# Performance work log

Measured on AMD Instinct MI355X. Metric: run time of the kernel, lower is better.

The kernel has to match this reference:

```python
import jax, jax.numpy as jnp
import numpy as np

B, N, C = 1, 4096, 1024
H = 16
HD = C // H  # head_dim = 64
SCALE = HD ** -0.5


def setup_inputs() -> dict:
    key = jax.random.key(0)
    k1, k2, k3, k4, k5 = jax.random.split(key, 5)
    x1 = jax.random.normal(k1, (B, N, C), dtype=jnp.float32)
    x2 = jax.random.normal(k2, (B, N, C), dtype=jnp.float32)
    # qkv: Linear(dim, 2*all_head_dim), bias=False. Stored as (in, out) for x @ W.
    W_qkv = jax.random.normal(k3, (C, 2 * H * HD), dtype=jnp.float32) * (C ** -0.5)
    # proj: Linear(all_head_dim, dim) with bias
    W_proj = jax.random.normal(k4, (H * HD, C), dtype=jnp.float32) * ((H * HD) ** -0.5)
    b_proj = jax.random.normal(k5, (C,), dtype=jnp.float32) * 0.01
    return {"x1": x1, "x2": x2, "W_qkv": W_qkv, "W_proj": W_proj, "b_proj": b_proj}


def reference(x1, x2, W_qkv, W_proj, b_proj):
    b, n, c = x1.shape
    # qk projection: (B,N,2*H*HD) -> (2,B,H,N,HD)
    qkv = (x1 @ W_qkv).reshape(b, n, 2, H, HD).transpose(2, 0, 3, 1, 4)
    q, k = qkv[0], qkv[1]  # (B,H,N,HD)
    # V2: reshape (N,1,H,HD) then permute -> (1,H,N,HD); valid since B==1
    v = x2.reshape(n, 1, H, HD).transpose(1, 2, 0, 3)
    attn = jax.nn.softmax(jnp.einsum('bhnd,bhmd->bhnm', q * SCALE, k), axis=-1)
    out = jnp.einsum('bhnm,bhmd->bhnd', attn, v)  # broadcasts v over batch
    out = out.transpose(0, 2, 1, 3).reshape(b, n, H * HD)
    return out @ W_proj + b_proj
```

## Files before the change

### kernel.cpp

```cpp
#include <hip/hip_runtime.h>

typedef unsigned short u16;
typedef unsigned int u32;

#define HNUM 16
#define NSEQ 4096
#define CDIM 1024
#define SCALE 0.125f
#define LOG2E 1.4426950408889634f

using bf16x8 = __attribute__((ext_vector_type(8))) __bf16;
using f32x4  = __attribute__((ext_vector_type(4))) float;
using u32x4  = __attribute__((ext_vector_type(4))) u32;

__device__ __forceinline__ u16 f2bf(float f) {
  union { float f; u32 u; } v; v.f = f;
  u32 u = v.u;
  return (u16)((u + 0x7fffu + ((u >> 16) & 1u)) >> 16);
}
__device__ __forceinline__ float fexp2(float x) { return __builtin_amdgcn_exp2f(x); }

__device__ __forceinline__ f32x4 mfma16(bf16x8 a, bf16x8 b, f32x4 c) {
  return __builtin_amdgcn_mfma_f32_16x16x32_bf16(a, b, c, 0, 0, 0);
}

__device__ __forceinline__ u32 pack2(float a, float b) {
  union { float f; u32 u; } A, B;
  A.f = a; B.f = b;
  return __builtin_amdgcn_perm(B.u + 0x8000u, A.u + 0x8000u, 0x07060302u);
}

__device__ __forceinline__ void g2l16(const void* g, void* l) {
  __builtin_amdgcn_global_load_lds(
      (const __attribute__((address_space(1))) unsigned int*)(unsigned long long)g,
      (__attribute__((address_space(3))) unsigned int*)(unsigned int)(unsigned long long)l,
      16, 0, 0);
}

__device__ __forceinline__ void cvtT_body(const float* __restrict__ in,
                                          u16* __restrict__ out, int R, int C,
                                          int bx, int by, float scale, int tid) {
  __shared__ u16 t[64][65];
  const int r0 = by * 64, c0 = bx * 64;
  const int tr = tid >> 2, tc = (tid & 3) * 16;
  const float* src = in + (r0 + tr) * C + c0 + tc;
#pragma unroll
  for (int i = 0; i < 16; ++i) t[tr][tc + i] = f2bf(src[i] * scale);
  __syncthreads();
  u16* dst = out + (c0 + tr) * R + r0 + tc;
#pragma unroll
  for (int i = 0; i < 16; ++i) dst[i] = t[tc + i][tr];
}

__global__ __launch_bounds__(256) void prep_k(const float* __restrict__ x1,
                                              u16* __restrict__ x1b,
                                              const float* __restrict__ Wqkv,
                                              u16* __restrict__ WqT,
                                              const float* __restrict__ Wproj,
                                              u16* __restrict__ WpT,
                                              const float* __restrict__ x2,
                                              u16* __restrict__ Vt,
                                              float cfac) {
  const int b = blockIdx.x, tid = threadIdx.x;
  if (b < 2048) {
    const int i = (b * 256 + tid) * 8;
    const float4 f0 = *(const float4*)(x1 + i);
    const float4 f1 = *(const float4*)(x1 + i + 4);
    u32 d[4] = {pack2(f0.x, f0.y), pack2(f0.z, f0.w),
                pack2(f1.x, f1.y), pack2(f1.z, f1.w)};
    *(bf16x8*)(x1b + i) = *(bf16x8*)d;
  } else if (b < 2560) {
    const int rel = b - 2048;
    const int bx = rel & 31, by = rel >> 5;
    cvtT_body(Wqkv, WqT, 1024, 2048, bx, by, bx < 16 ? cfac : 1.0f, tid);
  } else if (b < 2816) {
    const int rel = b - 2560;
    const int bx = rel & 15, by = rel >> 4;
    cvtT_body(Wproj, WpT, 1024, 1024, bx, by, 1.0f, tid);
  } else {
    const int rel = b - 2816;
    const int bx = rel & 15, by = rel >> 4;
    cvtT_body(x2, Vt, 4096, 1024, bx, by, 1.0f, tid);
  }
}

__global__ __launch_bounds__(256) void gemm1_k(const u16* __restrict__ A,
                                               const u16* __restrict__ Bt,
                                               u16* __restrict__ C,
                                               int M, int N, int K) {
  __shared__ __align__(16) u16 As[2][128 * 64];
  __shared__ __align__(16) u16 Bs[2][128 * 64];
  const int tid = threadIdx.x;
  const int wave = tid >> 6, lane = tid & 63;
  const int quad = lane >> 4, l16 = lane & 15;
  const int m0 = blockIdx.y * 128, n0 = blockIdx.x * 128;
  const int wm = wave * 32;
  const int lrow = lane >> 3, lc8 = (lane & 7) * 8;

  f32x4 acc[2][8] = {};
#pragma unroll
  for (int c = 0; c < 4; ++c) {
    const int cw = wave * 4 + c;
    g2l16(A + (m0 + cw * 8 + lrow) * K + lc8, (char*)As[0] + cw * 1024);
    g2l16(Bt + (n0 + cw * 8 + lrow) * K + lc8, (char*)Bs[0] + cw * 1024);
  }
  const int NIT = K / 64;
  for (int it = 0; it < NIT; ++it) {
    const int cur = it & 1;
    __syncthreads();
    if (it + 1 < NIT) {
      const int k0 = (it + 1) * 64;
#pragma unroll
      for (int c = 0; c < 4; ++c) {
        const int cw = wave * 4 + c;
        g2l16(A + (m0 + cw * 8 + lrow) * K + k0 + lc8, (char*)As[1 - cur] + cw * 1024);
        g2l16(Bt + (n0 + cw * 8 + lrow) * K + k0 + lc8, (char*)Bs[1 - cur] + cw * 1024);
      }
    }
#pragma unroll
    for (int ks = 0; ks < 2; ++ks) {
      bf16x8 a[2], b[8];
#pragma unroll
      for (int mt = 0; mt < 2; ++mt)
        a[mt] = *(const bf16x8*)(As[cur] + (wm + mt * 16 + l16) * 64 + ks * 32 + quad * 8);
#pragma unroll
      for (int nt = 0; nt < 8; ++nt)
        b[nt] = *(const bf16x8*)(Bs[cur] + (nt * 16 + l16) * 64 + ks * 32 + quad * 8);
#pragma unroll
      for (int mt = 0; mt < 2; ++mt)
#pragma unroll
        for (int nt = 0; nt < 8; ++nt)
          acc[mt][nt] = mfma16(a[mt], b[nt], acc[mt][nt]);
    }
  }
#pragma unroll
  for (int mt = 0; mt < 2; ++mt)
#pragma unroll
    for (int nt = 0; nt < 8; ++nt)
#pragma unroll
      for (int r = 0; r < 4; ++r)
        C[(m0 + wm + mt * 16 + quad * 4 + r) * N + n0 + nt * 16 + l16] =
            f2bf(acc[mt][nt][r]);
}

__global__ __launch_bounds__(256) void gemm2_k(const u16* __restrict__ A,
                                               const u16* __restrict__ Bt,
                                               float* __restrict__ C,
                                               const float* __restrict__ bias,
                                               int M, int N, int K) {
  __shared__ __align__(16) u16 As[2][128 * 64];
  __shared__ __align__(16) u16 Bs[2][64 * 64];
  const int tid = threadIdx.x;
  const int wave = tid >> 6, lane = tid & 63;
  const int quad = lane >> 4, l16 = lane & 15;
  const int m0 = blockIdx.y * 128, n0 = blockIdx.x * 64;
  const int wm = wave * 32;
  const int lrow = lane >> 3, lc8 = (lane & 7) * 8;

  f32x4 acc[2][4] = {};
#pragma unroll
  for (int c = 0; c < 4; ++c) {
    const int cw = wave * 4 + c;
    g2l16(A + (m0 + cw * 8 + lrow) * K + lc8, (char*)As[0] + cw * 1024);
  }
#pragma unroll
  for (int c = 0; c < 2; ++c) {
    const int cw = wave * 2 + c;
    g2l16(Bt + (n0 + cw * 8 + lrow) * K + lc8, (char*)Bs[0] + cw * 1024);
  }
  const int NIT = K / 64;
  for (int it = 0; it < NIT; ++it) {
    const int cur = it & 1;
    __syncthreads();
    if (it + 1 < NIT) {
      const int k0 = (it + 1) * 64;
#pragma unroll
      for (int c = 0; c < 4; ++c) {
        const int cw = wave * 4 + c;
        g2l16(A + (m0 + cw * 8 + lrow) * K + k0 + lc8, (char*)As[1 - cur] + cw * 1024);
      }
#pragma unroll
      for (int c = 0; c < 2; ++c) {
        const int cw = wave * 2 + c;
        g2l16(Bt + (n0 + cw * 8 + lrow) * K + k0 + lc8, (char*)Bs[1 - cur] + cw * 1024);
      }
    }
#pragma unroll
    for (int ks = 0; ks < 2; ++ks) {
      bf16x8 a[2], b[4];
#pragma unroll
      for (int mt = 0; mt < 2; ++mt)
        a[mt] = *(const bf16x8*)(As[cur] + (wm + mt * 16 + l16) * 64 + ks * 32 + quad * 8);
#pragma unroll
      for (int nt = 0; nt < 4; ++nt)
        b[nt] = *(const bf16x8*)(Bs[cur] + (nt * 16 + l16) * 64 + ks * 32 + quad * 8);
#pragma unroll
      for (int mt = 0; mt < 2; ++mt)
#pragma unroll
        for (int nt = 0; nt < 4; ++nt)
          acc[mt][nt] = mfma16(a[mt], b[nt], acc[mt][nt]);
    }
  }
#pragma unroll
  for (int mt = 0; mt < 2; ++mt)
#pragma unroll
    for (int nt = 0; nt < 4; ++nt)
#pragma unroll
      for (int r = 0; r < 4; ++r) {
        const int col = n0 + nt * 16 + l16;
        C[(m0 + wm + mt * 16 + quad * 4 + r) * N + col] = acc[mt][nt][r] + bias[col];
      }
}

__global__ __launch_bounds__(256) void attn_k(const u16* __restrict__ QK,
                                              const u16* __restrict__ Vt,
                                              u16* __restrict__ O) {
  __shared__ __align__(16) u16 Ks[2][64 * 64];
  __shared__ __align__(16) u16 Vs[2][64 * 64];
  __shared__ __align__(16) u16 Ps[4][32 * 64];
  const int tid = threadIdx.x;
  const int wave = tid >> 6, lane = tid & 63;
  const int quad = lane >> 4, l16 = lane & 15;
  const int head = blockIdx.y;
  const int qb = blockIdx.x * 128 + wave * 32;
  const int lrow = lane >> 3;
  const int lc8 = ((lane & 7) ^ lrow) * 8;
  const int swz = (quad ^ (l16 & 7)) * 8;

  const u16* kp[2];
  const u16* vp[2];
#pragma unroll
  for (int c = 0; c < 2; ++c) {
    const int row = (wave * 2 + c) * 8 + lrow;
    kp[c] = QK + row * 2048 + CDIM + head * 64 + lc8;
    vp[c] = Vt + (head * 64 + row) * NSEQ + lc8;
  }

  bf16x8 qf[2][2];
#pragma unroll
  for (int mt = 0; mt < 2; ++mt)
#pragma unroll
    for (int ks = 0; ks < 2; ++ks)
      qf[mt][ks] = *(const bf16x8*)(QK + (qb + mt * 16 + l16) * 2048 + head * 64 +
                                    ks * 32 + quad * 8);

  union { u32x4 u; bf16x8 b; } OU;
  OU.u = (u32x4){0x3F803F80u, 0x3F803F80u, 0x3F803F80u, 0x3F803F80u};
  const bf16x8 onesf = OU.b;

  f32x4 o[2][4] = {};
  f32x4 ol[2] = {};
  u16* Pw = Ps[wave];

#pragma unroll
  for (int c = 0; c < 2; ++c) {
    const int cw = wave * 2 + c;
    g2l16(kp[c], (char*)Ks[0] + cw * 1024);
    g2l16(vp[c], (char*)Vs[0] + cw * 1024);
    kp[c] += 64 * 2048;
    vp[c] += 64;
  }

  for (int kt = 0; kt < NSEQ / 64; ++kt) {
    const int cur = kt & 1;
    __syncthreads();

    if (kt < NSEQ / 64 - 1) {
#pragma unroll
      for (int c = 0; c < 2; ++c) {
        const int cw = wave * 2 + c;
        g2l16(kp[c], (char*)Ks[1 - cur] + cw * 1024);
        g2l16(vp[c], (char*)Vs[1 - cur] + cw * 1024);
        kp[c] += 64 * 2048;
        vp[c] += 64;
      }
    }

    const u16* Kc = Ks[cur];
    const u16* Vc = Vs[cur];

    f32x4 s[2][4] = {};
#pragma unroll
    for (int ks = 0; ks < 2; ++ks)
#pragma unroll
      for (int nt = 0; nt < 4; ++nt) {
        const bf16x8 kf =
            *(const bf16x8*)(Kc + (nt * 16 + l16) * 64 + (swz ^ (ks * 32)));
#pragma unroll
        for (int mt = 0; mt < 2; ++mt)
          s[mt][nt] = mfma16(kf, qf[mt][ks], s[mt][nt]);
      }

#pragma unroll
    for (int mt = 0; mt < 2; ++mt)
#pragma unroll
      for (int nt = 0; nt < 4; ++nt) {
        const float p0 = fexp2(s[mt][nt][0]);
        const float p1 = fexp2(s[mt][nt][1]);
        const float p2 = fexp2(s[mt][nt][2]);
        const float p3 = fexp2(s[mt][nt][3]);
        u32 d01 = pack2(p0, p1), d23 = pack2(p2, p3);
        const int col8 = (nt * 2 + (quad >> 1)) ^ (l16 & 7);
        u32* dst = (u32*)(Pw + (mt * 16 + l16) * 64 + col8 * 8 + (quad & 1) * 4);
        dst[0] = d01; dst[1] = d23;
      }

#pragma unroll
    for (int ks = 0; ks < 2; ++ks) {
      bf16x8 pf[2];
#pragma unroll
      for (int mt = 0; mt < 2; ++mt)
        pf[mt] = *(const bf16x8*)(Pw + (mt * 16 + l16) * 64 + (swz ^ (ks * 32)));
#pragma unroll
      for (int dt = 0; dt < 4; ++dt) {
        const bf16x8 vf =
            *(const bf16x8*)(Vc + (dt * 16 + l16) * 64 + (swz ^ (ks * 32)));
#pragma unroll
        for (int mt = 0; mt < 2; ++mt)
          o[mt][dt] = mfma16(pf[mt], vf, o[mt][dt]);
      }
#pragma unroll
      for (int mt = 0; mt < 2; ++mt)
        ol[mt] = mfma16(pf[mt], onesf, ol[mt]);
    }
  }

#pragma unroll
  for (int mt = 0; mt < 2; ++mt)
#pragma unroll
    for (int r = 0; r < 4; ++r) {
      const float lv = 1.0f / ol[mt][r];
#pragma unroll
      for (int dt = 0; dt < 4; ++dt)
        O[(qb + mt * 16 + quad * 4 + r) * CDIM + head * 64 + dt * 16 + l16] =
            f2bf(o[mt][dt][r] * lv);
    }
}

extern "C" void kernel_launch(void* const* d_in, const int* in_sizes, int n_in,
                              void* d_out, int out_size, void* d_ws, size_t ws_size,
                              hipStream_t stream) {
  const float* x1    = (const float*)d_in[0];
  const float* x2    = (const float*)d_in[1];
  const float* Wqkv  = (const float*)d_in[2];
  const float* Wproj = (const float*)d_in[3];
  const float* bproj = (const float*)d_in[4];
  float* out = (float*)d_out;

  char* ws = (char*)d_ws;
  u16* QK  = (u16*)(ws);
  u16* Vt  = (u16*)(ws + 16u * 1024 * 1024);
  u16* Obf = (u16*)(ws + 24u * 1024 * 1024);
  u16* WpT = (u16*)(ws + 32u * 1024 * 1024);
  u16* WqT = (u16*)(ws + 34u * 1024 * 1024);
  u16* x1b = (u16*)(ws + 38u * 1024 * 1024);

  const float cfac = SCALE * LOG2E;

  prep_k<<<dim3(3840), 256, 0, stream>>>(x1, x1b, Wqkv, WqT, Wproj, WpT, x2, Vt,
                                         cfac);
  gemm1_k<<<dim3(2048 / 128, 4096 / 128), 256, 0, stream>>>(x1b, WqT, QK,
                                                            4096, 2048, 1024);
  attn_k<<<dim3(4096 / 128, HNUM), 256, 0, stream>>>(QK, Vt, Obf);
  gemm2_k<<<dim3(1024 / 64, 4096 / 128), 256, 0, stream>>>(Obf, WpT, out, bproj,
                                                           4096, 1024, 1024);
}
```

Measured before the change: 228.2 us.

## Split attention over two KV halves and add a combine kernel

```diff
diff --git a/kernel.cpp b/kernel.cpp
--- a/kernel.cpp
+++ b/kernel.cpp
@@ -212,9 +212,11 @@
       }
 }
 
-__global__ __launch_bounds__(256) void attn_k(const u16* __restrict__ QK,
-                                              const u16* __restrict__ Vt,
-                                              u16* __restrict__ O) {
+__global__ __launch_bounds__(256) void attnsp_k(const u16* __restrict__ QK,
+                                                const u16* __restrict__ Vt,
+                                                u16* __restrict__ OP0,
+                                                u16* __restrict__ OP1,
+                                                float* __restrict__ LP) {
   __shared__ __align__(16) u16 Ks[2][64 * 64];
   __shared__ __align__(16) u16 Vs[2][64 * 64];
   __shared__ __align__(16) u16 Ps[4][32 * 64];
@@ -222,6 +224,7 @@
   const int wave = tid >> 6, lane = tid & 63;
   const int quad = lane >> 4, l16 = lane & 15;
   const int head = blockIdx.y;
+  const int z = blockIdx.z;
   const int qb = blockIdx.x * 128 + wave * 32;
   const int lrow = lane >> 3;
   const int lc8 = ((lane & 7) ^ lrow) * 8;
@@ -232,8 +235,8 @@
 #pragma unroll
   for (int c = 0; c < 2; ++c) {
     const int row = (wave * 2 + c) * 8 + lrow;
-    kp[c] = QK + row * 2048 + CDIM + head * 64 + lc8;
-    vp[c] = Vt + (head * 64 + row) * NSEQ + lc8;
+    kp[c] = QK + row * 2048 + CDIM + head * 64 + lc8 + z * (32 * 64 * 2048);
+    vp[c] = Vt + (head * 64 + row) * NSEQ + lc8 + z * (32 * 64);
   }
 
   bf16x8 qf[2][2];
@@ -261,11 +264,12 @@
     vp[c] += 64;
   }
 
-  for (int kt = 0; kt < NSEQ / 64; ++kt) {
+  const int NIT = NSEQ / 64 / 2;
+  for (int kt = 0; kt < NIT; ++kt) {
     const int cur = kt & 1;
     __syncthreads();
 
-    if (kt < NSEQ / 64 - 1) {
+    if (kt < NIT - 1) {
 #pragma unroll
       for (int c = 0; c < 2; ++c) {
         const int cw = wave * 2 + c;
@@ -325,16 +329,39 @@
     }
   }
 
+  u16* op = z ? OP1 : OP0;
+  float* lp = LP + (z * HNUM + head) * NSEQ;
 #pragma unroll
   for (int mt = 0; mt < 2; ++mt)
 #pragma unroll
     for (int r = 0; r < 4; ++r) {
-      const float lv = 1.0f / ol[mt][r];
+      const int row = qb + mt * 16 + quad * 4 + r;
+      if (l16 == 0) lp[row] = ol[mt][r];
 #pragma unroll
       for (int dt = 0; dt < 4; ++dt)
-        O[(qb + mt * 16 + quad * 4 + r) * CDIM + head * 64 + dt * 16 + l16] =
-            f2bf(o[mt][dt][r] * lv);
-    }
+        op[row * CDIM + head * 64 + dt * 16 + l16] = f2bf(o[mt][dt][r]);
+    }
+}
+
+__global__ __launch_bounds__(256) void comb_k(const u16* __restrict__ OP0,
+                                              const u16* __restrict__ OP1,
+                                              const float* __restrict__ LP,
+                                              u16* __restrict__ Obf) {
+  const int i = (blockIdx.x * 256 + threadIdx.x) * 8;
+  const int q = i >> 10;
+  const int head = (i >> 6) & (HNUM - 1);
+  const bf16x8 a = *(const bf16x8*)(OP0 + i);
+  const bf16x8 b = *(const bf16x8*)(OP1 + i);
+  const float inv =
+      1.0f / (LP[head * NSEQ + q] + LP[(HNUM + head) * NSEQ + q]);
+  u32 d[4];
+#pragma unroll
+  for (int j = 0; j < 4; ++j) {
+    const float f0 = ((float)a[2 * j] + (float)b[2 * j]) * inv;
+    const float f1 = ((float)a[2 * j + 1] + (float)b[2 * j + 1]) * inv;
+    d[j] = pack2(f0, f1);
+  }
+  *(bf16x8*)(Obf + i) = *(bf16x8*)d;
 }
 
 extern "C" void kernel_launch(void* const* d_in, const int* in_sizes, int n_in,
@@ -355,13 +382,18 @@
   u16* WqT = (u16*)(ws + 34u * 1024 * 1024);
   u16* x1b = (u16*)(ws + 38u * 1024 * 1024);
 
+  u16*   OP0 = x1b;
+  u16*   OP1 = Obf;
+  float* LP  = (float*)WqT;
+
   const float cfac = SCALE * LOG2E;
 
   prep_k<<<dim3(3840), 256, 0, stream>>>(x1, x1b, Wqkv, WqT, Wproj, WpT, x2, Vt,
                                          cfac);
   gemm1_k<<<dim3(2048 / 128, 4096 / 128), 256, 0, stream>>>(x1b, WqT, QK,
                                                             4096, 2048, 1024);
-  attn_k<<<dim3(4096 / 128, HNUM), 256, 0, stream>>>(QK, Vt, Obf);
+  attnsp_k<<<dim3(4096 / 128, HNUM, 2), 256, 0, stream>>>(QK, Vt, OP0, OP1, LP);
+  comb_k<<<dim3(NSEQ * CDIM / (256 * 8)), 256, 0, stream>>>(OP0, OP1, LP, Obf);
   gemm2_k<<<dim3(1024 / 64, 4096 / 128), 256, 0, stream>>>(Obf, WpT, out, bproj,
                                                            4096, 1024, 1024);
 }
```

Result: no change. 230.1 us (+0.8%).

## Load K and V fragments directly from global memory instead of LDS staging

Applied to the files above, without the earlier changes.

```diff
diff --git a/kernel.cpp b/kernel.cpp
--- a/kernel.cpp
+++ b/kernel.cpp
@@ -215,26 +215,13 @@
 __global__ __launch_bounds__(256) void attn_k(const u16* __restrict__ QK,
                                               const u16* __restrict__ Vt,
                                               u16* __restrict__ O) {
-  __shared__ __align__(16) u16 Ks[2][64 * 64];
-  __shared__ __align__(16) u16 Vs[2][64 * 64];
   __shared__ __align__(16) u16 Ps[4][32 * 64];
   const int tid = threadIdx.x;
   const int wave = tid >> 6, lane = tid & 63;
   const int quad = lane >> 4, l16 = lane & 15;
   const int head = blockIdx.y;
   const int qb = blockIdx.x * 128 + wave * 32;
-  const int lrow = lane >> 3;
-  const int lc8 = ((lane & 7) ^ lrow) * 8;
   const int swz = (quad ^ (l16 & 7)) * 8;
-
-  const u16* kp[2];
-  const u16* vp[2];
-#pragma unroll
-  for (int c = 0; c < 2; ++c) {
-    const int row = (wave * 2 + c) * 8 + lrow;
-    kp[c] = QK + row * 2048 + CDIM + head * 64 + lc8;
-    vp[c] = Vt + (head * 64 + row) * NSEQ + lc8;
-  }
 
   bf16x8 qf[2][2];
 #pragma unroll
@@ -248,36 +235,16 @@
   OU.u = (u32x4){0x3F803F80u, 0x3F803F80u, 0x3F803F80u, 0x3F803F80u};
   const bf16x8 onesf = OU.b;
 
+  const u16* Kg = QK + CDIM + head * 64;
+  const u16* Vg = Vt + (head * 64) * NSEQ;
+
   f32x4 o[2][4] = {};
   f32x4 ol[2] = {};
   u16* Pw = Ps[wave];
 
-#pragma unroll
-  for (int c = 0; c < 2; ++c) {
-    const int cw = wave * 2 + c;
-    g2l16(kp[c], (char*)Ks[0] + cw * 1024);
-    g2l16(vp[c], (char*)Vs[0] + cw * 1024);
-    kp[c] += 64 * 2048;
-    vp[c] += 64;
-  }
-
   for (int kt = 0; kt < NSEQ / 64; ++kt) {
-    const int cur = kt & 1;
-    __syncthreads();
-
-    if (kt < NSEQ / 64 - 1) {
-#pragma unroll
-      for (int c = 0; c < 2; ++c) {
-        const int cw = wave * 2 + c;
-        g2l16(kp[c], (char*)Ks[1 - cur] + cw * 1024);
-        g2l16(vp[c], (char*)Vs[1 - cur] + cw * 1024);
-        kp[c] += 64 * 2048;
-        vp[c] += 64;
-      }
-    }
-
-    const u16* Kc = Ks[cur];
-    const u16* Vc = Vs[cur];
+    const u16* Kt = Kg + kt * (64 * 2048);
+    const u16* Vc = Vg + kt * 64;
 
     f32x4 s[2][4] = {};
 #pragma unroll
@@ -285,7 +252,7 @@
 #pragma unroll
       for (int nt = 0; nt < 4; ++nt) {
         const bf16x8 kf =
-            *(const bf16x8*)(Kc + (nt * 16 + l16) * 64 + (swz ^ (ks * 32)));
+            *(const bf16x8*)(Kt + (nt * 16 + l16) * 2048 + ks * 32 + quad * 8);
 #pragma unroll
         for (int mt = 0; mt < 2; ++mt)
           s[mt][nt] = mfma16(kf, qf[mt][ks], s[mt][nt]);
@@ -314,7 +281,7 @@
 #pragma unroll
       for (int dt = 0; dt < 4; ++dt) {
         const bf16x8 vf =
-            *(const bf16x8*)(Vc + (dt * 16 + l16) * 64 + (swz ^ (ks * 32)));
+            *(const bf16x8*)(Vc + (dt * 16 + l16) * NSEQ + ks * 32 + quad * 8);
 #pragma unroll
         for (int mt = 0; mt < 2; ++mt)
           o[mt][dt] = mfma16(pf[mt], vf, o[mt][dt]);
```

Measured after the change: 439.4 us. 92.6% more time.
